# Kernel optimization log

Hardware: AMD Instinct MI355X
Metric: run time of the kernel (lower is better)

## Reference

```python
import jax, jax.numpy as jnp
import numpy as np

B = 65536          # batch
E = 512            # embedding_dim
SL = 128           # speed_latent_dim
H = 256            # hidden_size
NB = 6             # num_branch
D = E + SL         # 640, branch input dim


def _linear_init(k, din, dout):
    bound = 1.0 / np.sqrt(din)
    kw, kb = jax.random.split(k)
    W = jax.random.uniform(kw, (din, dout), minval=-bound, maxval=bound, dtype=jnp.float32)
    b = jax.random.uniform(kb, (dout,), minval=-bound, maxval=bound, dtype=jnp.float32)
    return W, b


def setup_inputs() -> dict:
    key = jax.random.key(0)
    ks = jax.random.split(key, 10)
    embedding = jax.random.normal(ks[0], (B, E), dtype=jnp.float32)
    speed = jax.random.uniform(ks[1], (B, 1), dtype=jnp.float32)
    command = jax.random.randint(ks[2], (B,), 1, NB + 1)  # values in 1..6

    # speed_in: Linear(1,H) -> ReLU -> Linear(H,SL)
    si_W1, si_b1 = _linear_init(ks[3], 1, H)
    si_W2, si_b2 = _linear_init(ks[4], H, SL)

    # speed_out: Linear(D,H) -> ReLU -> Linear(H,H) -> ReLU -> Linear(H,1)
    so_W1, so_b1 = _linear_init(ks[5], D, H)
    so_W2, so_b2 = _linear_init(ks[6], H, H)
    so_W3, so_b3 = _linear_init(ks[7], H, 1)

    # NB branches, each Linear(D,H)->ReLU->Linear(H,H)->ReLU->Linear(H,3)->Sigmoid
    def mk_branch(k):
        k1, k2, k3 = jax.random.split(k, 3)
        W1, b1 = _linear_init(k1, D, H)
        W2, b2 = _linear_init(k2, H, H)
        W3, b3 = _linear_init(k3, H, 3)
        return W1, b1, W2, b2, W3, b3

    bW1, bb1, bW2, bb2, bW3, bb3 = jax.vmap(mk_branch)(jax.random.split(ks[8], NB))

    return {
        "embedding": embedding, "speed": speed, "command": command,
        "si_W1": si_W1, "si_b1": si_b1, "si_W2": si_W2, "si_b2": si_b2,
        "bW1": bW1, "bb1": bb1, "bW2": bW2, "bb2": bb2, "bW3": bW3, "bb3": bb3,
        "so_W1": so_W1, "so_b1": so_b1, "so_W2": so_W2, "so_b2": so_b2,
        "so_W3": so_W3, "so_b3": so_b3,
    }


def reference(embedding, speed, command,
              si_W1, si_b1, si_W2, si_b2,
              bW1, bb1, bW2, bb2, bW3, bb3,
              so_W1, so_b1, so_W2, so_b2, so_W3, so_b3):
    # speed_in MLP and concat
    s = jax.nn.relu(speed @ si_W1 + si_b1) @ si_W2 + si_b2          # [B, SL]
    emb = jnp.concatenate([embedding, s], axis=1)                    # [B, D]

    # all branches computed densely (as in the torch module), then one-hot mask
    h1 = jax.nn.relu(jnp.einsum('bd,ndh->nbh', emb, bW1) + bb1[:, None, :])   # [NB,B,H]
    h2 = jax.nn.relu(jnp.einsum('nbh,nhk->nbk', h1, bW2) + bb2[:, None, :])   # [NB,B,H]
    out = jax.nn.sigmoid(jnp.einsum('nbk,nko->nbo', h2, bW3) + bb3[:, None, :])  # [NB,B,3]

    mask = (jnp.arange(NB)[:, None] == (command - 1)[None, :]).astype(out.dtype)  # [NB,B]
    control_pred = jnp.sum(out * mask[:, :, None], axis=0)           # [B, 3]

    # speed prediction head
    sp = jax.nn.relu(emb @ so_W1 + so_b1)
    sp = jax.nn.relu(sp @ so_W2 + so_b2)
    speed_pred = sp @ so_W3 + so_b3                                  # [B, 1]

    return control_pred, speed_pred
```

## Files before the change

kernel.cpp:

```cpp
#include <hip/hip_runtime.h>
#include <cstdint>
#include <cstddef>

typedef _Float16 f16;
typedef f16 f16x8 __attribute__((ext_vector_type(8)));
typedef float f32x4 __attribute__((ext_vector_type(4)));

#define B_ROWS 65536
#define TILE_M 128
#define NT_BRANCH 518
#define NT_SPEED 512

constexpr size_t OFF_AF16   = 0;
constexpr size_t SZ_AF16    = (size_t)B_ROWS * 640 * 2;
constexpr size_t OFF_SIW2T  = OFF_AF16 + SZ_AF16;
constexpr size_t SZ_SIW2T   = (size_t)128 * 256 * 2;
constexpr size_t OFF_BW1T   = OFF_SIW2T + SZ_SIW2T;
constexpr size_t SZ_BW1T    = (size_t)6 * 256 * 640 * 2;
constexpr size_t OFF_BW2T   = OFF_BW1T + SZ_BW1T;
constexpr size_t SZ_BW2T    = (size_t)6 * 256 * 256 * 2;
constexpr size_t OFF_SOW1T  = OFF_BW2T + SZ_BW2T;
constexpr size_t SZ_SOW1T   = (size_t)256 * 640 * 2;
constexpr size_t OFF_SOW2T  = OFF_SOW1T + SZ_SOW1T;
constexpr size_t SZ_SOW2T   = (size_t)256 * 256 * 2;
constexpr size_t OFF_BW3T16 = OFF_SOW2T + SZ_SOW2T;
constexpr size_t SZ_BW3T16  = (size_t)6 * 16 * 256 * 2;
constexpr size_t OFF_SOW3T16= OFF_BW3T16 + SZ_BW3T16;
constexpr size_t SZ_SOW3T16 = (size_t)16 * 256 * 2;
constexpr size_t OFF_COUNTS = OFF_SOW3T16 + SZ_SOW3T16;
constexpr size_t OFF_CURSORS= OFF_COUNTS + 256;
constexpr size_t OFF_BINBASE= OFF_CURSORS + 256;
constexpr size_t OFF_TILECMD= OFF_BINBASE + 256;
constexpr size_t OFF_PERM   = OFF_TILECMD + 4352;
constexpr size_t WS_NEEDED  = OFF_PERM + (size_t)NT_BRANCH * TILE_M * 4;

#define MFMA16(a, b, c) __builtin_amdgcn_mfma_f32_16x16x32_f16(a, b, c, 0, 0, 0)
#define BARSYNC() asm volatile("s_waitcnt lgkmcnt(0)\n\ts_barrier" ::: "memory")

__global__ void prep_kernel(const float* __restrict__ siW2,
                            const float* __restrict__ bW1,
                            const float* __restrict__ bW2,
                            const float* __restrict__ soW1,
                            const float* __restrict__ soW2,
                            const float* __restrict__ bW3,
                            const float* __restrict__ soW3,
                            f16* __restrict__ siW2T, f16* __restrict__ bW1T,
                            f16* __restrict__ bW2T, f16* __restrict__ soW1T,
                            f16* __restrict__ soW2T,
                            f16* __restrict__ bW3T16, f16* __restrict__ soW3T16,
                            int* __restrict__ counts, int* __restrict__ cursors,
                            int* __restrict__ perm)
{
    const int bx = blockIdx.x;
    const int tx = threadIdx.x, ty = threadIdx.y;
    const int tid = ty * 32 + tx;
    if (bx >= 1601) {
        const int ib = bx - 1601;
        const int idx = ib * 256 + tid;
        if (idx < NT_BRANCH * TILE_M) perm[idx] = -1;
        if (ib == 0 && tid < 6) { counts[tid] = 0; cursors[tid] = 0; }
        return;
    }
    if (bx == 1600) {
        for (int i = tid; i < 6 * 16 * 256; i += 256) {
            const int c = i >> 12, rem = i & 4095, n = rem >> 8, k = rem & 255;
            bW3T16[i] = (n < 3) ? (f16)bW3[((size_t)c * 256 + k) * 3 + n] : (f16)0;
        }
        for (int i = tid; i < 16 * 256; i += 256) {
            const int n = i >> 8, k = i & 255;
            soW3T16[i] = (n == 0) ? (f16)soW3[k] : (f16)0;
        }
        return;
    }
    const float* in; f16* out; int R, C, lb;
    if (bx < 960)       { int m = bx / 160;        lb = bx - m * 160;       in = bW1 + (size_t)m * 640 * 256; out = bW1T + (size_t)m * 640 * 256; R = 640; C = 256; }
    else if (bx < 1344) { int m = (bx - 960) / 64; lb = (bx - 960) - m * 64; in = bW2 + (size_t)m * 256 * 256; out = bW2T + (size_t)m * 256 * 256; R = 256; C = 256; }
    else if (bx < 1504) { lb = bx - 1344; in = soW1; out = soW1T; R = 640; C = 256; }
    else if (bx < 1568) { lb = bx - 1504; in = soW2; out = soW2T; R = 256; C = 256; }
    else                { lb = bx - 1568; in = siW2; out = siW2T; R = 256; C = 128; }
    const int txt = C >> 5;
    const int c0 = (lb % txt) << 5;
    const int r0 = (lb / txt) << 5;
    __shared__ float tile[32][33];
    #pragma unroll
    for (int i = 0; i < 4; ++i)
        tile[tx][ty + 8 * i] = in[(size_t)(r0 + ty + 8 * i) * C + c0 + tx];
    __syncthreads();
    #pragma unroll
    for (int i = 0; i < 4; ++i)
        out[(size_t)(c0 + ty + 8 * i) * R + r0 + tx] = (f16)tile[ty + 8 * i][tx];
}

__global__ __launch_bounds__(256) void speedin_kernel(
    const float* __restrict__ emb,
    const float* __restrict__ speed,
    const float* __restrict__ siW1, const float* __restrict__ sib1,
    const f16* __restrict__ siW2T, const float* __restrict__ sib2,
    const int* __restrict__ cmd,
    f16* __restrict__ AF16, int* __restrict__ counts)
{
    __shared__ f16 H[64 * 264];
    __shared__ float spd[64];
    __shared__ int h[6];
    const int tid = threadIdx.x;
    const int rb = blockIdx.x * 64;
    if (tid < 6) h[tid] = 0;
    __syncthreads();
    if (tid < 64) {
        spd[tid] = speed[rb + tid];
        atomicAdd(&h[cmd[rb + tid] - 1], 1);
    }
    __syncthreads();
    if (tid < 6 && h[tid] > 0) atomicAdd(&counts[tid], h[tid]);
    {
        const int rr = tid >> 2, pp = tid & 3;
        const float* src = emb + (size_t)(rb + rr) * 512 + pp * 128;
        f16* dst = AF16 + (size_t)(rb + rr) * 640 + pp * 128;
        #pragma unroll 4
        for (int i = 0; i < 16; ++i) {
            const float4 f0 = ((const float4*)src)[2 * i];
            const float4 f1 = ((const float4*)src)[2 * i + 1];
            f16x8 v;
            v[0] = (f16)f0.x; v[1] = (f16)f0.y; v[2] = (f16)f0.z; v[3] = (f16)f0.w;
            v[4] = (f16)f1.x; v[5] = (f16)f1.y; v[6] = (f16)f1.z; v[7] = (f16)f1.w;
            *(f16x8*)(dst + i * 8) = v;
        }
    }
    {
        const float w1 = siW1[tid], b1v = sib1[tid];
        #pragma unroll 4
        for (int r = 0; r < 64; ++r) {
            float hv = spd[r] * w1 + b1v;
            H[r * 264 + tid] = (f16)(hv > 0.f ? hv : 0.f);
        }
    }
    __syncthreads();
    const int w = tid >> 6, lane = tid & 63, lq = lane >> 4, l16 = lane & 15;
    const int nb = w * 32;
    f32x4 acc[4][2];
    #pragma unroll
    for (int mt = 0; mt < 4; ++mt)
        #pragma unroll
        for (int nt = 0; nt < 2; ++nt)
            acc[mt][nt] = (f32x4){0.f, 0.f, 0.f, 0.f};
    for (int ks = 0; ks < 8; ++ks) {
        const int koff = ks * 32 + lq * 8;
        f16x8 af[4], bf[2];
        #pragma unroll
        for (int mt = 0; mt < 4; ++mt)
            af[mt] = *(const f16x8*)(&H[(mt * 16 + l16) * 264 + koff]);
        #pragma unroll
        for (int nt = 0; nt < 2; ++nt)
            bf[nt] = *(const f16x8*)(siW2T + (size_t)(nb + nt * 16 + l16) * 256 + koff);
        #pragma unroll
        for (int mt = 0; mt < 4; ++mt)
            #pragma unroll
            for (int nt = 0; nt < 2; ++nt)
                acc[mt][nt] = MFMA16(af[mt], bf[nt], acc[mt][nt]);
    }
    #pragma unroll
    for (int mt = 0; mt < 4; ++mt)
        #pragma unroll
        for (int nt = 0; nt < 2; ++nt) {
            const int n = nb + nt * 16 + l16;
            const float bv = sib2[n];
            #pragma unroll
            for (int r2 = 0; r2 < 4; ++r2) {
                const int m = mt * 16 + lq * 4 + r2;
                AF16[(size_t)(rb + m) * 640 + 512 + n] = (f16)(acc[mt][nt][r2] + bv);
            }
        }
}

__global__ void plan_kernel(const int* __restrict__ counts,
                            int* __restrict__ binBase, int* __restrict__ tile_cmd) {
    __shared__ int tbase[7];
    if (threadIdx.x == 0) {
        int base = 0, tb = 0;
        for (int c = 0; c < 6; ++c) {
            binBase[c] = base;
            tbase[c] = tb;
            const int nt = (counts[c] + TILE_M - 1) >> 7;
            tb += nt;
            base += nt << 7;
        }
        tbase[6] = tb;
    }
    __syncthreads();
    for (int t = threadIdx.x; t < NT_BRANCH; t += 256) {
        int c = -1;
        #pragma unroll
        for (int j = 0; j < 6; ++j)
            if (t >= tbase[j] && t < tbase[j + 1]) c = j;
        tile_cmd[t] = c;
    }
}

__global__ void place_kernel(const int* __restrict__ cmd,
                             const int* __restrict__ binBase,
                             int* __restrict__ cursors, int* __restrict__ perm) {
    __shared__ int lcnt[6], lbase[6];
    const int tid = threadIdx.x;
    if (tid < 6) lcnt[tid] = 0;
    __syncthreads();
    const int i = blockIdx.x * 256 + tid;
    const int c = cmd[i] - 1;
    const int myr = atomicAdd(&lcnt[c], 1);
    __syncthreads();
    if (tid < 6) lbase[tid] = atomicAdd(&cursors[tid], lcnt[tid]);
    __syncthreads();
    perm[binBase[c] + lbase[c] + myr] = i;
}

__global__ __launch_bounds__(512, 3) void heads_kernel(
    const f16* __restrict__ AF16,
    const int* __restrict__ perm, const int* __restrict__ tile_cmd,
    const f16* __restrict__ bW1T, const f16* __restrict__ bW2T,
    const f16* __restrict__ bW3T16,
    const float* __restrict__ bb1, const float* __restrict__ bb2,
    const float* __restrict__ bb3,
    const f16* __restrict__ soW1T, const f16* __restrict__ soW2T,
    const f16* __restrict__ soW3T16,
    const float* __restrict__ sob1, const float* __restrict__ sob2,
    const float* __restrict__ sob3,
    float* __restrict__ out)
{
    __shared__ f16 smem[33792];
    __shared__ int rowIdx[TILE_M];
    const int bx = blockIdx.x;
    const int tid = threadIdx.x;
    const bool is_speed = (bx >= NT_BRANCH);
    const f16 *W1T, *W2T, *W3T;
    const float *bias1, *bias2, *bias3;
    if (is_speed) {
        const int t = bx - NT_BRANCH;
        if (tid < TILE_M) rowIdx[tid] = t * TILE_M + tid;
        W1T = soW1T; W2T = soW2T; W3T = soW3T16;
        bias1 = sob1; bias2 = sob2; bias3 = sob3;
    } else {
        const int c = tile_cmd[bx];
        if (c < 0) return;
        if (tid < TILE_M) rowIdx[tid] = perm[bx * TILE_M + tid];
        W1T = bW1T + (size_t)c * 256 * 640;
        W2T = bW2T + (size_t)c * 256 * 256;
        W3T = bW3T16 + (size_t)c * 16 * 256;
        bias1 = bb1 + c * 256; bias2 = bb2 + c * 256; bias3 = bb3 + c * 3;
    }
    __syncthreads();

    const int r = tid >> 2, p = tid & 3;
    int growS = rowIdx[r]; if (growS < 0) growS = 0;
    const f16* srcA = AF16 + (size_t)growS * 640 + p * 16;
    const int pOff = r * 72 + p * 16;

    const int w = tid >> 6, lane = tid & 63, lq = lane >> 4, l16 = lane & 15;
    const int nb = w * 32;
    const f16* brow0 = W1T + (size_t)(nb + l16) * 640;
    const f16* brow1 = W1T + (size_t)(nb + 16 + l16) * 640;

    f32x4 acc[8][2];
    #pragma unroll
    for (int mt = 0; mt < 8; ++mt)
        #pragma unroll
        for (int nt = 0; nt < 2; ++nt)
            acc[mt][nt] = (f32x4){0.f, 0.f, 0.f, 0.f};

    f16x8 sreg[4][2];
    #pragma unroll
    for (int j = 0; j < 4; ++j) {
        sreg[j][0] = ((const f16x8*)(srcA + j * 64))[0];
        sreg[j][1] = ((const f16x8*)(srcA + j * 64))[1];
    }
    f16x8 Bb[2][2];
    #pragma unroll
    for (int ks = 0; ks < 2; ++ks) {
        Bb[ks][0] = *(const f16x8*)(brow0 + ks * 32 + lq * 8);
        Bb[ks][1] = *(const f16x8*)(brow1 + ks * 32 + lq * 8);
    }
    *(f16x8*)(smem + pOff) = sreg[0][0];
    *(f16x8*)(smem + pOff + 8) = sreg[0][1];
    BARSYNC();

    #pragma unroll
    for (int kc = 0; kc < 10; ++kc) {
        const f16* cur = smem + (kc & 1) * 9216;
        if (kc < 9) {
            f16* dst = smem + ((kc + 1) & 1) * 9216 + pOff;
            *(f16x8*)(dst)     = sreg[(kc + 1) & 3][0];
            *(f16x8*)(dst + 8) = sreg[(kc + 1) & 3][1];
        }
        if (kc < 6) {
            sreg[kc & 3][0] = ((const f16x8*)(srcA + (kc + 4) * 64))[0];
            sreg[kc & 3][1] = ((const f16x8*)(srcA + (kc + 4) * 64))[1];
        }
        f16x8 Bn[2][2];
        if (kc < 9) {
            #pragma unroll
            for (int ks = 0; ks < 2; ++ks) {
                Bn[ks][0] = *(const f16x8*)(brow0 + (kc + 1) * 64 + ks * 32 + lq * 8);
                Bn[ks][1] = *(const f16x8*)(brow1 + (kc + 1) * 64 + ks * 32 + lq * 8);
            }
        }
        #pragma unroll
        for (int ks = 0; ks < 2; ++ks)
            #pragma unroll
            for (int mh = 0; mh < 2; ++mh) {
                f16x8 a[4];
                #pragma unroll
                for (int mt = 0; mt < 4; ++mt)
                    a[mt] = *(const f16x8*)(cur + ((mh * 4 + mt) * 16 + l16) * 72 + ks * 32 + lq * 8);
                #pragma unroll
                for (int mt = 0; mt < 4; ++mt) {
                    acc[mh * 4 + mt][0] = MFMA16(a[mt], Bb[ks][0], acc[mh * 4 + mt][0]);
                    acc[mh * 4 + mt][1] = MFMA16(a[mt], Bb[ks][1], acc[mh * 4 + mt][1]);
                }
            }
        if (kc < 9) {
            #pragma unroll
            for (int ks = 0; ks < 2; ++ks)
                #pragma unroll
                for (int nt = 0; nt < 2; ++nt)
                    Bb[ks][nt] = Bn[ks][nt];
        }
        BARSYNC();
    }

    const f16* brow2[2];
    #pragma unroll
    for (int nt = 0; nt < 2; ++nt)
        brow2[nt] = W2T + (size_t)(nb + nt * 16 + l16) * 256;
    f16x8 Bd[2][2];
    #pragma unroll
    for (int nt = 0; nt < 2; ++nt)
        Bd[0][nt] = *(const f16x8*)(brow2[nt] + lq * 8);

    #pragma unroll
    for (int mt = 0; mt < 8; ++mt)
        #pragma unroll
        for (int nt = 0; nt < 2; ++nt) {
            const int n = nb + nt * 16 + l16;
            const float bv = bias1[n];
            #pragma unroll
            for (int r2 = 0; r2 < 4; ++r2) {
                const int m = mt * 16 + lq * 4 + r2;
                const float v = acc[mt][nt][r2] + bv;
                smem[m * 264 + n] = (f16)(v > 0.f ? v : 0.f);
            }
            acc[mt][nt] = (f32x4){0.f, 0.f, 0.f, 0.f};
        }
    BARSYNC();

    #pragma unroll
    for (int ks = 0; ks < 8; ++ks) {
        if (ks < 7) {
            #pragma unroll
            for (int nt = 0; nt < 2; ++nt)
                Bd[(ks + 1) & 1][nt] = *(const f16x8*)(brow2[nt] + (ks + 1) * 32 + lq * 8);
        }
        #pragma unroll
        for (int mh = 0; mh < 2; ++mh) {
            f16x8 a[4];
            #pragma unroll
            for (int mt = 0; mt < 4; ++mt)
                a[mt] = *(const f16x8*)(&smem[((mh * 4 + mt) * 16 + l16) * 264 + ks * 32 + lq * 8]);
            #pragma unroll
            for (int mt = 0; mt < 4; ++mt) {
                acc[mh * 4 + mt][0] = MFMA16(a[mt], Bd[ks & 1][0], acc[mh * 4 + mt][0]);
                acc[mh * 4 + mt][1] = MFMA16(a[mt], Bd[ks & 1][1], acc[mh * 4 + mt][1]);
            }
        }
    }
    BARSYNC();
    #pragma unroll
    for (int mt = 0; mt < 8; ++mt)
        #pragma unroll
        for (int nt = 0; nt < 2; ++nt) {
            const int n = nb + nt * 16 + l16;
            const float bv = bias2[n];
            #pragma unroll
            for (int r2 = 0; r2 < 4; ++r2) {
                const int m = mt * 16 + lq * 4 + r2;
                const float v = acc[mt][nt][r2] + bv;
                smem[m * 264 + n] = (f16)(v > 0.f ? v : 0.f);
            }
        }
    BARSYNC();
    {
        f32x4 acc3 = (f32x4){0.f, 0.f, 0.f, 0.f};
        const f16* w3row = W3T + (size_t)l16 * 256;
        #pragma unroll
        for (int ks = 0; ks < 8; ++ks) {
            const int koff = ks * 32 + lq * 8;
            const f16x8 af = *(const f16x8*)(&smem[(w * 16 + l16) * 264 + koff]);
            const f16x8 bf = *(const f16x8*)(w3row + koff);
            acc3 = MFMA16(af, bf, acc3);
        }
        const int orow = w * 16 + lq * 4;
        if (!is_speed) {
            if (l16 < 3) {
                const float b3 = bias3[l16];
                #pragma unroll
                for (int r2 = 0; r2 < 4; ++r2) {
                    const int g = rowIdx[orow + r2];
                    if (g >= 0)
                        out[(size_t)g * 3 + l16] = 1.f / (1.f + __expf(-(acc3[r2] + b3)));
                }
            }
        } else {
            if (l16 == 0) {
                const float b3 = bias3[0];
                #pragma unroll
                for (int r2 = 0; r2 < 4; ++r2) {
                    const int g = rowIdx[orow + r2];
                    if (g >= 0)
                        out[(size_t)3 * B_ROWS + g] = acc3[r2] + b3;
                }
            }
        }
    }
}

extern "C" void kernel_launch(void* const* d_in, const int* in_sizes, int n_in,
                              void* d_out, int out_size, void* d_ws, size_t ws_size,
                              hipStream_t stream) {
    (void)in_sizes; (void)n_in; (void)out_size; (void)ws_size;
    const float* embedding = (const float*)d_in[0];
    const float* speed     = (const float*)d_in[1];
    const int*   command   = (const int*)d_in[2];
    const float* si_W1 = (const float*)d_in[3];
    const float* si_b1 = (const float*)d_in[4];
    const float* si_W2 = (const float*)d_in[5];
    const float* si_b2 = (const float*)d_in[6];
    const float* bW1   = (const float*)d_in[7];
    const float* bb1   = (const float*)d_in[8];
    const float* bW2   = (const float*)d_in[9];
    const float* bb2   = (const float*)d_in[10];
    const float* bW3   = (const float*)d_in[11];
    const float* bb3   = (const float*)d_in[12];
    const float* so_W1 = (const float*)d_in[13];
    const float* so_b1 = (const float*)d_in[14];
    const float* so_W2 = (const float*)d_in[15];
    const float* so_b2 = (const float*)d_in[16];
    const float* so_W3 = (const float*)d_in[17];
    const float* so_b3 = (const float*)d_in[18];
    float* out = (float*)d_out;

    char* ws = (char*)d_ws;
    f16* AF16   = (f16*)(ws + OFF_AF16);
    f16* siW2T  = (f16*)(ws + OFF_SIW2T);
    f16* bW1T   = (f16*)(ws + OFF_BW1T);
    f16* bW2T   = (f16*)(ws + OFF_BW2T);
    f16* soW1T  = (f16*)(ws + OFF_SOW1T);
    f16* soW2T  = (f16*)(ws + OFF_SOW2T);
    f16* bW3T16 = (f16*)(ws + OFF_BW3T16);
    f16* soW3T16= (f16*)(ws + OFF_SOW3T16);
    int* counts = (int*)(ws + OFF_COUNTS);
    int* cursors= (int*)(ws + OFF_CURSORS);
    int* binBase= (int*)(ws + OFF_BINBASE);
    int* tile_cmd = (int*)(ws + OFF_TILECMD);
    int* perm   = (int*)(ws + OFF_PERM);

    prep_kernel<<<1860, dim3(32, 8), 0, stream>>>(
        si_W2, bW1, bW2, so_W1, so_W2, bW3, so_W3,
        siW2T, bW1T, bW2T, soW1T, soW2T, bW3T16, soW3T16,
        counts, cursors, perm);
    speedin_kernel<<<1024, 256, 0, stream>>>(
        embedding, speed, si_W1, si_b1, siW2T, si_b2, command, AF16, counts);
    plan_kernel<<<1, 256, 0, stream>>>(counts, binBase, tile_cmd);
    place_kernel<<<256, 256, 0, stream>>>(command, binBase, cursors, perm);
    heads_kernel<<<NT_BRANCH + NT_SPEED, 512, 0, stream>>>(
        AF16, perm, tile_cmd,
        bW1T, bW2T, bW3T16, bb1, bb2, bb3,
        soW1T, soW2T, soW3T16, so_b1, so_b2, so_b3, out);
}
```

Before: 392.0 us.

## Stream A tiles directly to LDS with triple-buffered swizzled global_load_lds

The first-layer GEMM loop in heads_kernel now uses global_load_lds to copy A rows straight into a three-stage XOR-swizzled LDS ring, replacing the register-staged double buffer. This removes the VGPR staging and the ds_write work, and lets occupancy be raised to 4 blocks per CU. B fragments are now loaded at the start of each iteration instead of being prefetched one step ahead. The pre-pass embedding conversion is also reorganised so that a wavefront reads whole contiguous rows for coalescing. The vmcnt-based waits depend on exact in-flight load counts, which could race if the compiler reorders the B loads.

```diff
diff --git a/kernel.cpp b/kernel.cpp
--- a/kernel.cpp
+++ b/kernel.cpp
@@ -36,6 +36,9 @@
 
 #define MFMA16(a, b, c) __builtin_amdgcn_mfma_f32_16x16x32_f16(a, b, c, 0, 0, 0)
 #define BARSYNC() asm volatile("s_waitcnt lgkmcnt(0)\n\ts_barrier" ::: "memory")
+#define GLOAD16(gp, lp) __builtin_amdgcn_global_load_lds( \
+    (const __attribute__((address_space(1))) void*)(gp),  \
+    (__attribute__((address_space(3))) void*)(lp), 16, 0, 0)
 
 __global__ void prep_kernel(const float* __restrict__ siW2,
                             const float* __restrict__ bW1,
@@ -113,17 +116,17 @@
     __syncthreads();
     if (tid < 6 && h[tid] > 0) atomicAdd(&counts[tid], h[tid]);
     {
-        const int rr = tid >> 2, pp = tid & 3;
-        const float* src = emb + (size_t)(rb + rr) * 512 + pp * 128;
-        f16* dst = AF16 + (size_t)(rb + rr) * 640 + pp * 128;
+        const int wv = tid >> 6, ln = tid & 63;
         #pragma unroll 4
-        for (int i = 0; i < 16; ++i) {
-            const float4 f0 = ((const float4*)src)[2 * i];
-            const float4 f1 = ((const float4*)src)[2 * i + 1];
+        for (int rr = 0; rr < 16; ++rr) {
+            const int row = rb + wv * 16 + rr;
+            const float* src = emb + (size_t)row * 512 + ln * 8;
+            const float4 f0 = ((const float4*)src)[0];
+            const float4 f1 = ((const float4*)src)[1];
             f16x8 v;
             v[0] = (f16)f0.x; v[1] = (f16)f0.y; v[2] = (f16)f0.z; v[3] = (f16)f0.w;
             v[4] = (f16)f1.x; v[5] = (f16)f1.y; v[6] = (f16)f1.z; v[7] = (f16)f1.w;
-            *(f16x8*)(dst + i * 8) = v;
+            *(f16x8*)(AF16 + (size_t)row * 640 + ln * 8) = v;
         }
     }
     {
@@ -212,7 +215,7 @@
     perm[binBase[c] + lbase[c] + myr] = i;
 }
 
-__global__ __launch_bounds__(512, 3) void heads_kernel(
+__global__ __launch_bounds__(512, 4) void heads_kernel(
     const f16* __restrict__ AF16,
     const int* __restrict__ perm, const int* __restrict__ tile_cmd,
     const f16* __restrict__ bW1T, const f16* __restrict__ bW2T,
@@ -248,12 +251,14 @@
     }
     __syncthreads();
 
-    const int r = tid >> 2, p = tid & 3;
-    int growS = rowIdx[r]; if (growS < 0) growS = 0;
-    const f16* srcA = AF16 + (size_t)growS * 640 + p * 16;
-    const int pOff = r * 72 + p * 16;
+    const int r0 = tid >> 3, j = tid & 7, key = r0 & 7;
+    int g0 = rowIdx[r0];      if (g0 < 0) g0 = 0;
+    int g1 = rowIdx[r0 + 64]; if (g1 < 0) g1 = 0;
+    const f16* srcP0 = AF16 + (size_t)g0 * 640 + (j ^ key) * 8;
+    const f16* srcP1 = AF16 + (size_t)g1 * 640 + (j ^ key) * 8;
 
     const int w = tid >> 6, lane = tid & 63, lq = lane >> 4, l16 = lane & 15;
+    const int ldsW = w * 512;
     const int nb = w * 32;
     const f16* brow0 = W1T + (size_t)(nb + l16) * 640;
     const f16* brow1 = W1T + (size_t)(nb + 16 + l16) * 640;
@@ -265,41 +270,24 @@
         for (int nt = 0; nt < 2; ++nt)
             acc[mt][nt] = (f32x4){0.f, 0.f, 0.f, 0.f};
 
-    f16x8 sreg[4][2];
-    #pragma unroll
-    for (int j = 0; j < 4; ++j) {
-        sreg[j][0] = ((const f16x8*)(srcA + j * 64))[0];
-        sreg[j][1] = ((const f16x8*)(srcA + j * 64))[1];
-    }
-    f16x8 Bb[2][2];
-    #pragma unroll
-    for (int ks = 0; ks < 2; ++ks) {
-        Bb[ks][0] = *(const f16x8*)(brow0 + ks * 32 + lq * 8);
-        Bb[ks][1] = *(const f16x8*)(brow1 + ks * 32 + lq * 8);
-    }
-    *(f16x8*)(smem + pOff) = sreg[0][0];
-    *(f16x8*)(smem + pOff + 8) = sreg[0][1];
-    BARSYNC();
+    GLOAD16(srcP0,            smem + 0 * 8192 + ldsW);
+    GLOAD16(srcP1,            smem + 0 * 8192 + 4096 + ldsW);
+    GLOAD16(srcP0 + 64,       smem + 1 * 8192 + ldsW);
+    GLOAD16(srcP1 + 64,       smem + 1 * 8192 + 4096 + ldsW);
+    asm volatile("s_waitcnt vmcnt(2)\n\ts_barrier" ::: "memory");
 
     #pragma unroll
     for (int kc = 0; kc < 10; ++kc) {
-        const f16* cur = smem + (kc & 1) * 9216;
-        if (kc < 9) {
-            f16* dst = smem + ((kc + 1) & 1) * 9216 + pOff;
-            *(f16x8*)(dst)     = sreg[(kc + 1) & 3][0];
-            *(f16x8*)(dst + 8) = sreg[(kc + 1) & 3][1];
-        }
-        if (kc < 6) {
-            sreg[kc & 3][0] = ((const f16x8*)(srcA + (kc + 4) * 64))[0];
-            sreg[kc & 3][1] = ((const f16x8*)(srcA + (kc + 4) * 64))[1];
-        }
-        f16x8 Bn[2][2];
-        if (kc < 9) {
-            #pragma unroll
-            for (int ks = 0; ks < 2; ++ks) {
-                Bn[ks][0] = *(const f16x8*)(brow0 + (kc + 1) * 64 + ks * 32 + lq * 8);
-                Bn[ks][1] = *(const f16x8*)(brow1 + (kc + 1) * 64 + ks * 32 + lq * 8);
-            }
+        const f16* cur = smem + (kc % 3) * 8192;
+        f16x8 Bb[2][2];
+        #pragma unroll
+        for (int ks = 0; ks < 2; ++ks) {
+            Bb[ks][0] = *(const f16x8*)(brow0 + kc * 64 + ks * 32 + lq * 8);
+            Bb[ks][1] = *(const f16x8*)(brow1 + kc * 64 + ks * 32 + lq * 8);
+        }
+        if (kc < 8) {
+            GLOAD16(srcP0 + (kc + 2) * 64, smem + ((kc + 2) % 3) * 8192 + ldsW);
+            GLOAD16(srcP1 + (kc + 2) * 64, smem + ((kc + 2) % 3) * 8192 + 4096 + ldsW);
         }
         #pragma unroll
         for (int ks = 0; ks < 2; ++ks)
@@ -307,22 +295,22 @@
             for (int mh = 0; mh < 2; ++mh) {
                 f16x8 a[4];
                 #pragma unroll
-                for (int mt = 0; mt < 4; ++mt)
-                    a[mt] = *(const f16x8*)(cur + ((mh * 4 + mt) * 16 + l16) * 72 + ks * 32 + lq * 8);
+                for (int mt = 0; mt < 4; ++mt) {
+                    const int row = mh * 64 + mt * 16 + l16;
+                    a[mt] = *(const f16x8*)(cur + row * 64 + ((ks * 4 + lq) ^ (l16 & 7)) * 8);
+                }
                 #pragma unroll
                 for (int mt = 0; mt < 4; ++mt) {
                     acc[mh * 4 + mt][0] = MFMA16(a[mt], Bb[ks][0], acc[mh * 4 + mt][0]);
                     acc[mh * 4 + mt][1] = MFMA16(a[mt], Bb[ks][1], acc[mh * 4 + mt][1]);
                 }
             }
-        if (kc < 9) {
-            #pragma unroll
-            for (int ks = 0; ks < 2; ++ks)
-                #pragma unroll
-                for (int nt = 0; nt < 2; ++nt)
-                    Bb[ks][nt] = Bn[ks][nt];
-        }
-        BARSYNC();
+        if (kc < 8)
+            asm volatile("s_waitcnt vmcnt(2)\n\ts_barrier" ::: "memory");
+        else if (kc == 8)
+            asm volatile("s_waitcnt vmcnt(4)\n\ts_barrier" ::: "memory");
+        else
+            BARSYNC();
     }
 
     const f16* brow2[2];
```

New measurement: 405.9 us. 3.5% more time.
